# Kernel optimization log

Measured on AMD Instinct MI355X. Metric: run time of the kernel, lower is better.

Reference implementation:

```python
import jax, jax.numpy as jnp
import numpy as np
import math

NEG_INF = -1000000000.0
D_EMBED = 1024
D_K = 1024
N_HEADS = 16
D_H = D_EMBED // N_HEADS


def setup_inputs() -> dict:
    key = jax.random.key(0)
    ks = jax.random.split(key, 12)
    B, S = 2, 2048
    s = 0.02
    return {
        "embed": jax.random.normal(ks[0], (B, S, D_EMBED), dtype=jnp.float32),
        "key": jax.random.normal(ks[1], (B, S, D_K), dtype=jnp.float32),
        "attn_mask": jax.random.randint(ks[2], (B, S, S), 0, 2, dtype=jnp.int32),
        "Wq": jax.random.normal(ks[3], (D_EMBED, D_EMBED), dtype=jnp.float32) * s,
        "bq": jnp.zeros((D_EMBED,), dtype=jnp.float32),
        "Wk": jax.random.normal(ks[4], (D_EMBED, D_K), dtype=jnp.float32) * s,
        "bk": jnp.zeros((D_EMBED,), dtype=jnp.float32),
        "Wv": jax.random.normal(ks[5], (D_EMBED, D_K), dtype=jnp.float32) * s,
        "bv": jnp.zeros((D_EMBED,), dtype=jnp.float32),
        "Wo": jax.random.normal(ks[6], (D_EMBED, D_EMBED), dtype=jnp.float32) * s,
        "bo": jnp.zeros((D_EMBED,), dtype=jnp.float32),
    }


def _alibi_bias(seq_len: int, n_heads: int) -> jnp.ndarray:
    # symmetric |i-j| distances, slopes 2^-(8k/H) for k=1..H
    r = jnp.arange(seq_len)
    pos = jnp.abs(r[None, :] - r[:, None]).astype(jnp.float32)  # [S, S]
    step = 8.0 / n_heads
    ms = 2.0 ** (-jnp.arange(step, 8.0 + step, step, dtype=jnp.float32))  # [H]
    return ms[:, None, None] * pos[None, :, :]  # [H, S, S]


def reference(embed, key, attn_mask, Wq, bq, Wk, bk, Wv, bv, Wo, bo):
    B, Sq, _ = embed.shape
    Sk = key.shape[1]
    Q = embed @ Wq.T + bq          # [B, Sq, D]
    K = key @ Wk.T + bk            # [B, Sk, D]
    V = key @ Wv.T + bv            # [B, Sk, D]
    Qh = Q.reshape(B, Sq, N_HEADS, D_H).transpose(0, 2, 1, 3)  # [B, H, Sq, d_h]
    Kh = K.reshape(B, Sk, N_HEADS, D_H).transpose(0, 2, 1, 3)
    Vh = V.reshape(B, Sk, N_HEADS, D_H).transpose(0, 2, 1, 3)
    attn = jnp.einsum("bhqd,bhkd->bhqk", Qh, Kh)
    # ALiBi bias subtracted BEFORE scaling (as in source)
    attn = attn - _alibi_bias(Sq, N_HEADS)[None]
    attn = attn * (1.0 / math.sqrt(D_EMBED))  # note: scale uses d_embed, not d_h
    attn = jnp.where(attn_mask[:, None, :, :] == 0, NEG_INF, attn)
    attn = jax.nn.softmax(attn, axis=-1)
    out = jnp.einsum("bhqk,bhkd->bhqd", attn, Vh)
    out = out.transpose(0, 2, 1, 3).reshape(B, Sq, D_EMBED)
    return out @ Wo.T + bo
```

## Files before the change

### kernel.cpp

```cpp
#include <hip/hip_runtime.h>


typedef _Float16 f16;
typedef __attribute__((ext_vector_type(8))) _Float16 f16x8;
typedef __attribute__((ext_vector_type(4))) _Float16 f16x4;
typedef __attribute__((ext_vector_type(4))) float f32x4;
typedef unsigned long long u64;
typedef unsigned int u32;

#define MFMA16 __builtin_amdgcn_mfma_f32_16x16x32_f16
#define MFMA16K16 __builtin_amdgcn_mfma_f32_16x16x16f16

__device__ __forceinline__ void gl16(const f16* g, f16* l) {
    __builtin_amdgcn_global_load_lds(
        (const __attribute__((address_space(1))) void*)(const void*)g,
        (__attribute__((address_space(3))) void*)(void*)l,
        16, 0, 0);
}

__global__ __launch_bounds__(256) void k_convert(
    const float* __restrict__ embed, const float* __restrict__ key,
    const float* __restrict__ wq, const float* __restrict__ wk,
    const float* __restrict__ wv, const float* __restrict__ wo,
    f16* __restrict__ xe, f16* __restrict__ xk,
    f16* __restrict__ wqh, f16* __restrict__ wkh,
    f16* __restrict__ wvh, f16* __restrict__ woh)
{
    long g = (long)blockIdx.x * 256 + threadIdx.x;
    const float* src; f16* dst; long off;
    if (g < 524288)       { src = embed; dst = xe; off = g; }
    else if (g < 1048576) { src = key;   dst = xk; off = g - 524288; }
    else {
        long t = g - 1048576; int wi = (int)(t >> 17); off = t & 131071;
        if (wi == 0)      { src = wq; dst = wqh; }
        else if (wi == 1) { src = wk; dst = wkh; }
        else if (wi == 2) { src = wv; dst = wvh; }
        else              { src = wo; dst = woh; }
    }
    const float4* s4 = (const float4*)src;
    float4 a = s4[off * 2], b = s4[off * 2 + 1];
    f16x8 o;
    o[0]=(f16)a.x; o[1]=(f16)a.y; o[2]=(f16)a.z; o[3]=(f16)a.w;
    o[4]=(f16)b.x; o[5]=(f16)b.y; o[6]=(f16)b.z; o[7]=(f16)b.w;
    *(f16x8*)(dst + off * 8) = o;
}

__global__ __launch_bounds__(256) void k_packmask(
    const int* __restrict__ mask, u64* __restrict__ bits)
{
    int gw = (blockIdx.x * 256 + threadIdx.x) >> 6;
    int lane = threadIdx.x & 63;
    const int* row = mask + (long)gw * 2048;
    u64* out = bits + (long)gw * 32;
    #pragma unroll 4
    for (int c = 0; c < 32; ++c) {
        int v = row[c * 64 + lane];
        u64 b = __ballot(v != 0);
        if (lane == 0) out[c] = b;
    }
}

__global__ __launch_bounds__(256) void k_qkv(
    const f16* __restrict__ xe, const f16* __restrict__ xk,
    const f16* __restrict__ wqh, const f16* __restrict__ wkh, const f16* __restrict__ wvh,
    const float* __restrict__ bq, const float* __restrict__ bk, const float* __restrict__ bv,
    f16* __restrict__ Qh, f16* __restrict__ Kh, f16* __restrict__ Vt)
{
    int bid = blockIdx.x;
    int which = bid >> 8;
    int rr_ = bid & 255;
    int tm = rr_ >> 3, tn = rr_ & 7;
    const f16* X = (which == 0) ? xe : xk;
    const f16* W = (which == 0) ? wqh : (which == 1) ? wkh : wvh;
    const float* bias = (which == 0) ? bq : (which == 1) ? bk : bv;

    __shared__ f16 smem[128 * 136];
    f16* la = smem;
    f16* lb = smem + 128 * 64;

    int tid = threadIdx.x;
    int lane = tid & 63, wid = tid >> 6;
    int wr = wid >> 1, wc = wid & 1;
    int lm = lane & 15, qd = lane >> 4;

    f32x4 acc[4][4];
    #pragma unroll
    for (int i = 0; i < 4; i++)
        #pragma unroll
        for (int j = 0; j < 4; j++) acc[i][j] = (f32x4)0.0f;

    int m0 = tm * 128, n0 = tn * 128;

    for (int kt = 0; kt < 16; ++kt) {
        int k0 = kt * 64;
        __syncthreads();
        #pragma unroll
        for (int t = 0; t < 4; ++t) {
            int cid = tid + t * 256;
            int row = cid >> 3;
            int cg = cid & 7;
            int sw = cg ^ (row & 7);
            *(f16x8*)&la[row * 64 + sw * 8] =
                *(const f16x8*)&X[(long)(m0 + row) * 1024 + k0 + cg * 8];
            *(f16x8*)&lb[row * 64 + sw * 8] =
                *(const f16x8*)&W[(long)(n0 + row) * 1024 + k0 + cg * 8];
        }
        __syncthreads();
        #pragma unroll
        for (int ks = 0; ks < 2; ++ks) {
            f16x8 af[4], bfr[4];
            #pragma unroll
            for (int i = 0; i < 4; i++) {
                int m = 64 * wr + 16 * i + lm;
                int g = (ks * 4 + qd) ^ (m & 7);
                af[i] = *(const f16x8*)&la[m * 64 + g * 8];
                int n = 64 * wc + 16 * i + lm;
                int g2 = (ks * 4 + qd) ^ (n & 7);
                bfr[i] = *(const f16x8*)&lb[n * 64 + g2 * 8];
            }
            #pragma unroll
            for (int i = 0; i < 4; i++)
                #pragma unroll
                for (int j = 0; j < 4; j++)
                    acc[i][j] = MFMA16(af[i], bfr[j], acc[i][j], 0, 0, 0);
        }
    }

    if (which == 2) {
        #pragma unroll
        for (int j = 0; j < 4; j++) {
            int n = n0 + 64 * wc + 16 * j + lm;
            float bb = bias[n];
            int h = n >> 6, d = n & 63;
            #pragma unroll
            for (int i = 0; i < 4; i++) {
                int mbase = m0 + 64 * wr + 16 * i + 4 * qd;
                f16x4 pk;
                #pragma unroll
                for (int r = 0; r < 4; ++r) pk[r] = (f16)(acc[i][j][r] + bb);
                int b = mbase >> 11, s = mbase & 2047;
                *(f16x4*)&Vt[(((long)(b * 16 + h)) * 64 + d) * 2048 + s] = pk;
            }
        }
    } else {
        f16* dst = (which == 0) ? Qh : Kh;
        float sc = (which == 0) ? 0.0450842252f : 1.0f;
        __syncthreads();
        #pragma unroll
        for (int j = 0; j < 4; j++) {
            int col = 64 * wc + 16 * j + lm;
            float bb = bias[n0 + col];
            #pragma unroll
            for (int i = 0; i < 4; i++) {
                int row = 64 * wr + 16 * i + 4 * qd;
                #pragma unroll
                for (int r = 0; r < 4; ++r)
                    smem[(row + r) * 136 + col] = (f16)((acc[i][j][r] + bb) * sc);
            }
        }
        __syncthreads();
        #pragma unroll
        for (int t = 0; t < 8; ++t) {
            int ci = tid + t * 256;
            int row = ci >> 4, cg = ci & 15;
            f16x8 v = *(const f16x8*)&smem[row * 136 + cg * 8];
            int m = m0 + row;
            int b = m >> 11, s = m & 2047;
            int h = (n0 >> 6) + (cg >> 3);
            int d0 = (cg & 7) * 8;
            *(f16x8*)&dst[(((long)(b * 16 + h)) * 2048 + s) * 64 + d0] = v;
        }
    }
}

__global__ __launch_bounds__(512, 4) void k_attn(
    const f16* __restrict__ Qh, const f16* __restrict__ Kh, const f16* __restrict__ Vt,
    const u64* __restrict__ mbits, f16* __restrict__ O)
{
    int bid = blockIdx.x;
    int qt = bid & 15;
    int h = (bid >> 4) & 15;
    int b = bid >> 8;
    int q0 = qt * 128;

    const f16* Qg = Qh + ((long)(b * 16 + h)) * 2048 * 64;
    const f16* Kg = Kh + ((long)(b * 16 + h)) * 2048 * 64;
    const f16* Vg = Vt + ((long)(b * 16 + h)) * 64 * 2048;

    __shared__ f16 smem[32768];

    int tid = threadIdx.x, lane = tid & 63, wid = tid >> 6;
    int lm = lane & 15, qd = lane >> 4;
    int qs = wid & 3;
    int hf = wid >> 2;

    int qb = q0 + 32 * qs;
    const u64* Mrow0 = mbits + ((long)(b * 2048) + qb + lm) * 32;
    const u64* Mrow1 = mbits + ((long)(b * 2048) + qb + 16 + lm) * 32;

    int bi = wid >> 1, sub = wid & 1;
    f16* ldst = smem + bi * 8192 + sub * 4096;
    const f16* gE; const f16* gO; long gstep;
    if (bi < 2) {
        int krow0 = sub * 64 + (lane >> 3);
        int kcg = (lane & 7) ^ (krow0 & 7);
        gE = Kg + ((long)bi * 1024 + krow0) * 64 + kcg * 8;
        gO = gE + 512;
        gstep = 1024;
    } else {
        int vh = bi - 2;
        int vrow0 = sub * 32 + (lane >> 4);
        int vgE = (lane & 15) ^ (vrow0 & 7);
        gE = Vg + (long)vrow0 * 2048 + vh * 1024 + vgE * 8;
        gO = Vg + (long)(vrow0 + 4) * 2048 + vh * 1024 + (vgE ^ 4) * 8;
        gstep = 16384;
    }
    long giter = (bi < 2) ? (long)128 * 64 : 128;

    const f16* ksH = smem + hf * 8192;
    const f16* vsH = smem + 16384 + hf * 8192;

    f16x8 aq[2][2];
    #pragma unroll
    for (int g = 0; g < 2; ++g)
        #pragma unroll
        for (int ksi = 0; ksi < 2; ++ksi)
            aq[g][ksi] = *(const f16x8*)&Qg[(long)(qb + 16 * g + lm) * 64 + ksi * 32 + qd * 8];

    f32x4 oacc[2][4], lacc[2];
    #pragma unroll
    for (int g = 0; g < 2; ++g) {
        #pragma unroll
        for (int c = 0; c < 4; c++) oacc[g][c] = (f32x4)0.0f;
        lacc[g] = (f32x4)0.0f;
    }
    f16x4 vone4;
    #pragma unroll
    for (int j = 0; j < 4; j++) vone4[j] = (f16)1.0f;

    float negc2 = -__builtin_amdgcn_exp2f(-0.5f * (float)(h + 1)) * 0.0450842252f;

    int vgq = qd >> 1;
    int off4 = (qd & 1) * 4;
    int shb = 4 * qd;

    for (int it = 0; it < 8; ++it) {
        __syncthreads();
        #pragma unroll
        for (int p = 0; p < 4; ++p) {
            gl16(gE + p * gstep, ldst + (2 * p) * 512);
            gl16(gO + p * gstep, ldst + (2 * p + 1) * 512);
        }
        gE += giter; gO += giter;
        __syncthreads();

        int kt = hf * 8 + it;
        u64 w0a = Mrow0[kt * 2], w1a = Mrow0[kt * 2 + 1];
        u64 w0b = Mrow1[kt * 2], w1b = Mrow1[kt * 2 + 1];

        float qmk0 = (float)(qb + lm - kt * 128 - 4 * qd);
        float qmk1 = qmk0 + 16.0f;

        #pragma unroll
        for (int c = 0; c < 8; ++c) {
            int kr = 16 * c + lm;
            f32x4 s0 = (f32x4)0.0f, s1 = (f32x4)0.0f;
            #pragma unroll
            for (int ksi = 0; ksi < 2; ++ksi) {
                int gg = (ksi * 4 + qd) ^ (kr & 7);
                f16x8 ak = *(const f16x8*)&ksH[kr * 64 + gg * 8];
                s0 = MFMA16(ak, aq[0][ksi], s0, 0, 0, 0);
                s1 = MFMA16(ak, aq[1][ksi], s1, 0, 0, 0);
            }
            u32 niba = (u32)(((c < 4) ? w0a : w1a) >> (16 * (c & 3) + shb)) & 15u;
            u32 nibb = (u32)(((c < 4) ? w0b : w1b) >> (16 * (c & 3) + shb)) & 15u;
            float qc0 = qmk0 - 16.0f * (float)c;
            float qc1 = qmk1 - 16.0f * (float)c;
            f16x4 pk0, pk1;
            #pragma unroll
            for (int r = 0; r < 4; ++r) {
                float u0 = fmaf(fabsf(qc0 - (float)r), negc2, s0[r]);
                u0 = ((niba >> r) & 1u) ? u0 : -1e30f;
                pk0[r] = (f16)__builtin_amdgcn_exp2f(u0);
                float u1 = fmaf(fabsf(qc1 - (float)r), negc2, s1[r]);
                u1 = ((nibb >> r) & 1u) ? u1 : -1e30f;
                pk1[r] = (f16)__builtin_amdgcn_exp2f(u1);
            }
            int vgc = 2 * c + vgq;
            #pragma unroll
            for (int cc = 0; cc < 4; ++cc) {
                int d = 16 * cc + lm;
                f16x4 vb = *(const f16x4*)&vsH[d * 128 + (vgc ^ (d & 7)) * 8 + off4];
                oacc[0][cc] = MFMA16K16(pk0, vb, oacc[0][cc], 0, 0, 0);
                oacc[1][cc] = MFMA16K16(pk1, vb, oacc[1][cc], 0, 0, 0);
            }
            lacc[0] = MFMA16K16(pk0, vone4, lacc[0], 0, 0, 0);
            lacc[1] = MFMA16K16(pk1, vone4, lacc[1], 0, 0, 0);
        }
    }

    __syncthreads();
    float* cO = (float*)smem;
    float* lL = (float*)(smem + 16384);
    f16*  fO  = smem + 16640;

    if (hf == 1) {
        #pragma unroll
        for (int g = 0; g < 2; ++g) {
            #pragma unroll
            for (int cc = 0; cc < 4; ++cc)
                #pragma unroll
                for (int r = 0; r < 4; ++r)
                    cO[(qs * 32 + 16 * g + 4 * qd + r) * 64 + 16 * cc + lm] = oacc[g][cc][r];
            if (lm == 0) {
                #pragma unroll
                for (int r = 0; r < 4; ++r)
                    lL[qs * 32 + 16 * g + 4 * qd + r] = lacc[g][r];
            }
        }
    }
    __syncthreads();
    if (hf == 0) {
        #pragma unroll
        for (int g = 0; g < 2; ++g) {
            float linv[4];
            #pragma unroll
            for (int r = 0; r < 4; ++r)
                linv[r] = 1.0f / fmaxf(lacc[g][r] + lL[qs * 32 + 16 * g + 4 * qd + r], 1e-30f);
            #pragma unroll
            for (int cc = 0; cc < 4; ++cc)
                #pragma unroll
                for (int r = 0; r < 4; ++r) {
                    int idx = (qs * 32 + 16 * g + 4 * qd + r) * 64 + 16 * cc + lm;
                    fO[idx] = (f16)((oacc[g][cc][r] + cO[idx]) * linv[r]);
                }
        }
    }
    __syncthreads();
    #pragma unroll
    for (int t = 0; t < 2; ++t) {
        int ci = tid + t * 512;
        int q = ci >> 3, dc = ci & 7;
        f16x8 v = *(const f16x8*)&fO[q * 64 + dc * 8];
        *(f16x8*)&O[((long)(b * 2048 + q0 + q)) * 1024 + h * 64 + dc * 8] = v;
    }
}

__global__ __launch_bounds__(256) void k_proj(
    const f16* __restrict__ Oh, const f16* __restrict__ woh,
    const float* __restrict__ bo, float* __restrict__ out)
{
    int bid = blockIdx.x;
    int tm = bid >> 3, tn = bid & 7;

    __shared__ f16 la[128 * 64];
    __shared__ f16 lb[128 * 64];

    int tid = threadIdx.x;
    int lane = tid & 63, wid = tid >> 6;
    int wr = wid >> 1, wc = wid & 1;
    int lm = lane & 15, qd = lane >> 4;

    f32x4 acc[4][4];
    #pragma unroll
    for (int i = 0; i < 4; i++)
        #pragma unroll
        for (int j = 0; j < 4; j++) acc[i][j] = (f32x4)0.0f;

    int m0 = tm * 128, n0 = tn * 128;

    for (int kt = 0; kt < 16; ++kt) {
        int k0 = kt * 64;
        __syncthreads();
        #pragma unroll
        for (int t = 0; t < 4; ++t) {
            int cid = tid + t * 256;
            int row = cid >> 3;
            int cg = cid & 7;
            int sw = cg ^ (row & 7);
            *(f16x8*)&la[row * 64 + sw * 8] =
                *(const f16x8*)&Oh[(long)(m0 + row) * 1024 + k0 + cg * 8];
            *(f16x8*)&lb[row * 64 + sw * 8] =
                *(const f16x8*)&woh[(long)(n0 + row) * 1024 + k0 + cg * 8];
        }
        __syncthreads();
        #pragma unroll
        for (int ks = 0; ks < 2; ++ks) {
            f16x8 af[4], bfr[4];
            #pragma unroll
            for (int i = 0; i < 4; i++) {
                int m = 64 * wr + 16 * i + lm;
                int g = (ks * 4 + qd) ^ (m & 7);
                af[i] = *(const f16x8*)&la[m * 64 + g * 8];
                int n = 64 * wc + 16 * i + lm;
                int g2 = (ks * 4 + qd) ^ (n & 7);
                bfr[i] = *(const f16x8*)&lb[n * 64 + g2 * 8];
            }
            #pragma unroll
            for (int i = 0; i < 4; i++)
                #pragma unroll
                for (int j = 0; j < 4; j++)
                    acc[i][j] = MFMA16(af[i], bfr[j], acc[i][j], 0, 0, 0);
        }
    }

    #pragma unroll
    for (int j = 0; j < 4; j++) {
        int n = n0 + 64 * wc + 16 * j + lm;
        float bb = bo[n];
        #pragma unroll
        for (int i = 0; i < 4; i++) {
            int mbase = m0 + 64 * wr + 16 * i + 4 * qd;
            #pragma unroll
            for (int r = 0; r < 4; ++r)
                out[(long)(mbase + r) * 1024 + n] = acc[i][j][r] + bb;
        }
    }
}

extern "C" void kernel_launch(void* const* d_in, const int* in_sizes, int n_in,
                              void* d_out, int out_size, void* d_ws, size_t ws_size,
                              hipStream_t stream)
{
    const float* embed = (const float*)d_in[0];
    const float* key   = (const float*)d_in[1];
    const int*   mask  = (const int*)d_in[2];
    const float* Wq = (const float*)d_in[3];
    const float* bq = (const float*)d_in[4];
    const float* Wk = (const float*)d_in[5];
    const float* bk = (const float*)d_in[6];
    const float* Wv = (const float*)d_in[7];
    const float* bv = (const float*)d_in[8];
    const float* Wo = (const float*)d_in[9];
    const float* bo = (const float*)d_in[10];

    char* ws = (char*)d_ws;
    f16* xe  = (f16*)(ws + 0);
    f16* xk  = (f16*)(ws + 8388608);
    f16* wqh = (f16*)(ws + 16777216);
    f16* wkh = (f16*)(ws + 18874368);
    f16* wvh = (f16*)(ws + 20971520);
    f16* woh = (f16*)(ws + 23068672);
    f16* Qh  = (f16*)(ws + 25165824);
    f16* Kh  = (f16*)(ws + 33554432);
    f16* Vt  = (f16*)(ws + 41943040);
    f16* Oh  = (f16*)(ws + 50331648);
    u64* mb  = (u64*)(ws + 58720256);
    float* out = (float*)d_out;

    k_convert<<<6144, 256, 0, stream>>>(embed, key, Wq, Wk, Wv, Wo,
                                        xe, xk, wqh, wkh, wvh, woh);
    k_packmask<<<1024, 256, 0, stream>>>(mask, mb);
    k_qkv<<<768, 256, 0, stream>>>(xe, xk, wqh, wkh, wvh, bq, bk, bv, Qh, Kh, Vt);
    k_attn<<<512, 512, 0, stream>>>(Qh, Kh, Vt, mb, Oh);
    k_proj<<<256, 256, 0, stream>>>(Oh, woh, bo, out);
}
```

Baseline: 287.3 us.

## Double-buffer attention K/V tiles, remap block order, and raise MFMA priority

The attention kernel now stages K/V in 64-key tiles across two LDS buffers. The next tile's global-to-LDS load is issued before computing on the current one, leaving one barrier per iteration instead of two with an exposed load. Block IDs are remapped so neighbouring workgroups land on different heads/batches, and s_setprio is raised around MFMA groups in the attention and both GEMM kernels to favour matrix issue. Smaller tiles double the iteration count and barrier frequency, and the priority hints may not help scheduling.

```diff
diff --git a/kernel.cpp b/kernel.cpp
--- a/kernel.cpp
+++ b/kernel.cpp
@@ -118,11 +118,13 @@
                 int g2 = (ks * 4 + qd) ^ (n & 7);
                 bfr[i] = *(const f16x8*)&lb[n * 64 + g2 * 8];
             }
+            __builtin_amdgcn_s_setprio(1);
             #pragma unroll
             for (int i = 0; i < 4; i++)
                 #pragma unroll
                 for (int j = 0; j < 4; j++)
                     acc[i][j] = MFMA16(af[i], bfr[j], acc[i][j], 0, 0, 0);
+            __builtin_amdgcn_s_setprio(0);
         }
     }
 
@@ -177,7 +179,8 @@
     const f16* __restrict__ Qh, const f16* __restrict__ Kh, const f16* __restrict__ Vt,
     const u64* __restrict__ mbits, f16* __restrict__ O)
 {
-    int bid = blockIdx.x;
+    int bid0 = blockIdx.x;
+    int bid = (bid0 & 7) * 64 + (bid0 >> 3);
     int qt = bid & 15;
     int h = (bid >> 4) & 15;
     int b = bid >> 8;
@@ -196,29 +199,33 @@
 
     int qb = q0 + 32 * qs;
     const u64* Mrow0 = mbits + ((long)(b * 2048) + qb + lm) * 32;
-    const u64* Mrow1 = mbits + ((long)(b * 2048) + qb + 16 + lm) * 32;
+    const u64* Mrow1 = Mrow0 + 16 * 32;
 
     int bi = wid >> 1, sub = wid & 1;
-    f16* ldst = smem + bi * 8192 + sub * 4096;
-    const f16* gE; const f16* gO; long gstep;
+    int rowL = lane >> 3;
+    int cgL = (lane & 7) ^ rowL;
+    const f16* gsrc; long lstep, istep; int doff;
     if (bi < 2) {
-        int krow0 = sub * 64 + (lane >> 3);
-        int kcg = (lane & 7) ^ (krow0 & 7);
-        gE = Kg + ((long)bi * 1024 + krow0) * 64 + kcg * 8;
-        gO = gE + 512;
-        gstep = 1024;
+        gsrc = Kg + ((long)(bi * 1024 + sub * 32 + rowL)) * 64 + cgL * 8;
+        lstep = 512;
+        istep = 4096;
+        doff = bi * 4096 + sub * 2048;
     } else {
         int vh = bi - 2;
-        int vrow0 = sub * 32 + (lane >> 4);
-        int vgE = (lane & 15) ^ (vrow0 & 7);
-        gE = Vg + (long)vrow0 * 2048 + vh * 1024 + vgE * 8;
-        gO = Vg + (long)(vrow0 + 4) * 2048 + vh * 1024 + (vgE ^ 4) * 8;
-        gstep = 16384;
-    }
-    long giter = (bi < 2) ? (long)128 * 64 : 128;
-
-    const f16* ksH = smem + hf * 8192;
-    const f16* vsH = smem + 16384 + hf * 8192;
+        gsrc = Vg + ((long)(sub * 32 + rowL)) * 2048 + vh * 1024 + cgL * 8;
+        lstep = 16384;
+        istep = 64;
+        doff = 8192 + vh * 4096 + sub * 2048;
+    }
+
+    #define ATTN_STAGE(pb, it)                                                 \
+        {                                                                      \
+            f16* d0 = smem + (pb) * 16384 + doff;                              \
+            const f16* s0_ = gsrc + (it) * istep;                              \
+            _Pragma("unroll")                                                  \
+            for (int li = 0; li < 4; ++li)                                     \
+                gl16(s0_ + li * lstep, d0 + li * 512);                         \
+        }
 
     f16x8 aq[2][2];
     #pragma unroll
@@ -242,29 +249,27 @@
 
     int vgq = qd >> 1;
     int off4 = (qd & 1) * 4;
-    int shb = 4 * qd;
-
-    for (int it = 0; it < 8; ++it) {
-        __syncthreads();
-        #pragma unroll
-        for (int p = 0; p < 4; ++p) {
-            gl16(gE + p * gstep, ldst + (2 * p) * 512);
-            gl16(gO + p * gstep, ldst + (2 * p + 1) * 512);
-        }
-        gE += giter; gO += giter;
-        __syncthreads();
-
-        int kt = hf * 8 + it;
-        u64 w0a = Mrow0[kt * 2], w1a = Mrow0[kt * 2 + 1];
-        u64 w0b = Mrow1[kt * 2], w1b = Mrow1[kt * 2 + 1];
-
-        float qmk0 = (float)(qb + lm - kt * 128 - 4 * qd);
+
+    ATTN_STAGE(0, 0);
+    __syncthreads();
+
+    for (int it = 0; it < 16; ++it) {
+        int pb = it & 1;
+        if (it < 15) ATTN_STAGE(pb ^ 1, it + 1);
+
+        const f16* ksH = smem + pb * 16384 + hf * 4096;
+        const f16* vsH = smem + pb * 16384 + 8192 + hf * 4096;
+
+        u64 wa = Mrow0[hf * 16 + it];
+        u64 wb = Mrow1[hf * 16 + it];
+        float qmk0 = (float)(qb + lm - hf * 1024 - it * 64 - 4 * qd);
         float qmk1 = qmk0 + 16.0f;
 
         #pragma unroll
-        for (int c = 0; c < 8; ++c) {
+        for (int c = 0; c < 4; ++c) {
             int kr = 16 * c + lm;
             f32x4 s0 = (f32x4)0.0f, s1 = (f32x4)0.0f;
+            __builtin_amdgcn_s_setprio(1);
             #pragma unroll
             for (int ksi = 0; ksi < 2; ++ksi) {
                 int gg = (ksi * 4 + qd) ^ (kr & 7);
@@ -272,8 +277,9 @@
                 s0 = MFMA16(ak, aq[0][ksi], s0, 0, 0, 0);
                 s1 = MFMA16(ak, aq[1][ksi], s1, 0, 0, 0);
             }
-            u32 niba = (u32)(((c < 4) ? w0a : w1a) >> (16 * (c & 3) + shb)) & 15u;
-            u32 nibb = (u32)(((c < 4) ? w0b : w1b) >> (16 * (c & 3) + shb)) & 15u;
+            __builtin_amdgcn_s_setprio(0);
+            u32 niba = (u32)(wa >> (16 * c + 4 * qd)) & 15u;
+            u32 nibb = (u32)(wb >> (16 * c + 4 * qd)) & 15u;
             float qc0 = qmk0 - 16.0f * (float)c;
             float qc1 = qmk1 - 16.0f * (float)c;
             f16x4 pk0, pk1;
@@ -287,19 +293,22 @@
                 pk1[r] = (f16)__builtin_amdgcn_exp2f(u1);
             }
             int vgc = 2 * c + vgq;
+            __builtin_amdgcn_s_setprio(1);
             #pragma unroll
             for (int cc = 0; cc < 4; ++cc) {
                 int d = 16 * cc + lm;
-                f16x4 vb = *(const f16x4*)&vsH[d * 128 + (vgc ^ (d & 7)) * 8 + off4];
+                f16x4 vb = *(const f16x4*)&vsH[d * 64 + (vgc ^ (d & 7)) * 8 + off4];
                 oacc[0][cc] = MFMA16K16(pk0, vb, oacc[0][cc], 0, 0, 0);
                 oacc[1][cc] = MFMA16K16(pk1, vb, oacc[1][cc], 0, 0, 0);
             }
             lacc[0] = MFMA16K16(pk0, vone4, lacc[0], 0, 0, 0);
             lacc[1] = MFMA16K16(pk1, vone4, lacc[1], 0, 0, 0);
-        }
-    }
-
-    __syncthreads();
+            __builtin_amdgcn_s_setprio(0);
+        }
+        __syncthreads();
+    }
+    #undef ATTN_STAGE
+
     float* cO = (float*)smem;
     float* lL = (float*)(smem + 16384);
     f16*  fO  = smem + 16640;
@@ -396,11 +405,13 @@
                 int g2 = (ks * 4 + qd) ^ (n & 7);
                 bfr[i] = *(const f16x8*)&lb[n * 64 + g2 * 8];
             }
+            __builtin_amdgcn_s_setprio(1);
             #pragma unroll
             for (int i = 0; i < 4; i++)
                 #pragma unroll
                 for (int j = 0; j < 4; j++)
                     acc[i][j] = MFMA16(af[i], bfr[j], acc[i][j], 0, 0, 0);
+            __builtin_amdgcn_s_setprio(0);
         }
     }
 
```

Measured after the change: 277.1 us. 1.04x faster.
